# Optimization experiments

Measured on AMD Instinct MI355X. Metric: run time of the kernel, lower is better.

The kernel has to match this reference:

```python
import jax, jax.numpy as jnp
import numpy as np

B = 256      # number of graphs
IN = 128     # input_dim
FD = 256     # feature_dim (dims[1])
HID = 256    # hidden_dim of attention block (dims[2])
OUT = 128    # final output dim (dims[3])
TXT = 512    # text_emb_dim

LENGTHS = np.asarray(128 + (np.arange(B) % 256), dtype=np.int64)  # ragged lens 128..383
N = int(LENGTHS.sum())  # 65408 total nodes
LMAX = int(LENGTHS.max())  # 383


def setup_inputs() -> dict:
    key = jax.random.key(0)
    ks = jax.random.split(key, 16)
    s = 0.02
    return {
        "input": jax.random.normal(ks[0], (N, IN), jnp.float32),
        "text_emb": jax.random.normal(ks[1], (B, TXT), jnp.float32),
        "repeat_list": jnp.asarray(LENGTHS),
        # layer 0: Linear(IN -> FD)
        "W0": jax.random.normal(ks[2], (IN, FD), jnp.float32) * s,
        "b0": jax.random.normal(ks[3], (FD,), jnp.float32) * s,
        # cross-attention block params
        "Wq": jax.random.normal(ks[4], (TXT, FD), jnp.float32) * s,
        "bq": jax.random.normal(ks[5], (FD,), jnp.float32) * s,
        "Wk": jax.random.normal(ks[6], (FD, FD), jnp.float32) * s,
        "bk": jax.random.normal(ks[7], (FD,), jnp.float32) * s,
        "Wv": jax.random.normal(ks[8], (FD, FD), jnp.float32) * s,
        "bv": jax.random.normal(ks[9], (FD,), jnp.float32) * s,
        "Wo": jax.random.normal(ks[10], (FD, HID), jnp.float32) * s,
        "bo": jax.random.normal(ks[11], (HID,), jnp.float32) * s,
        # layer 2: Linear(HID -> OUT), last layer (no activation)
        "W2": jax.random.normal(ks[12], (HID, OUT), jnp.float32) * s,
        "b2": jax.random.normal(ks[13], (OUT,), jnp.float32) * s,
    }


def _cross_attention(h, text_emb, repeat_list, Wq, bq, Wk, bk, Wv, bv, Wo, bo):
    # h: [N, FD] packed ragged node features; repeat_list: [B] lengths (constant ints)
    n = h.shape[0]
    b = repeat_list.shape[0]
    fd = h.shape[1]
    # pad ragged -> [B, LMAX, FD] (pad value 0) + validity mask
    seg = jnp.repeat(jnp.arange(b), repeat_list, total_repeat_length=n)  # [N] graph id
    offsets = jnp.cumsum(repeat_list) - repeat_list                      # [B] start of each graph
    pos = jnp.arange(n) - offsets[seg]                                   # [N] within-graph pos
    padded = jnp.zeros((b, LMAX, fd), h.dtype).at[seg, pos].set(h)
    valid = jnp.arange(LMAX)[None, :] < repeat_list[:, None]             # [B, L]

    q = text_emb @ Wq + bq                              # [B, FD]
    k = (padded @ Wk + bk) * valid[..., None]           # masked_fill(mask==0, 0)
    v = (padded @ Wv + bv) * valid[..., None]

    # query is broadcast identically over the padded-length axis, so each row of the
    # [L, L] score matrix is the same vector: scores[b, j] = q[b] . k[b, j]
    scores = jnp.einsum('bf,bjf->bj', q, k)             # [B, L]
    scores = jnp.where(valid, scores, -jnp.inf)         # mask invalid columns j
    p = jax.nn.softmax(scores, axis=-1)                 # [B, L]
    # output = attention^T @ value with identical rows => out[b,j,:] = p[b,j] * sum_i v[b,i,:]
    v_sum = v.sum(axis=1)                               # [B, FD] (padded rows already zero)
    out_pad = p[..., None] * v_sum[:, None, :]          # [B, L, FD]
    out_nodes = out_pad[seg, pos]                       # unpad-concat -> [N, FD]
    return out_nodes @ Wo + bo                          # [N, HID]


def reference(input, text_emb, repeat_list, W0, b0, Wq, bq, Wk, bk, Wv, bv, Wo, bo, W2, b2):
    h = jax.nn.relu(input @ W0 + b0)                                     # layer 0 + relu
    h = _cross_attention(h, text_emb, repeat_list, Wq, bq, Wk, bk, Wv, bv, Wo, bo)
    h = jax.nn.relu(h)                                                   # layer 1 + relu
    return h @ W2 + b2                                                   # layer 2 (last, no act)
```

## Files before the change

### kernel.cpp

```cpp
#include <hip/hip_runtime.h>
#include <math.h>

#define B_G   256
#define IN_D  128
#define FD    256
#define HID   256
#define OUT_D 128
#define TXT   512
#define XKS   136
#define ZKS   72

typedef short bf16x8 __attribute__((ext_vector_type(8)));
typedef float f32x4  __attribute__((ext_vector_type(4)));

__device__ __forceinline__ unsigned bf_rne(float x) {
    unsigned u = __float_as_uint(x);
    u += 0x7fffu + ((u >> 16) & 1u);
    return u >> 16;
}
__device__ __forceinline__ float bf_to_f(unsigned h) {
    return __uint_as_float(h << 16);
}
__device__ __forceinline__ void split2(float a0, float a1, unsigned& hp, unsigned& lp) {
    unsigned h0 = bf_rne(a0), h1 = bf_rne(a1);
    float r0 = a0 - bf_to_f(h0), r1 = a1 - bf_to_f(h1);
    hp = h0 | (h1 << 16);
    lp = bf_rne(r0) | (bf_rne(r1) << 16);
}

__global__ __launch_bounds__(256) void k_prepA(
    const float* __restrict__ text_emb, const float* __restrict__ Wq,
    const float* __restrict__ bq, const float* __restrict__ Wk,
    const float* __restrict__ W0, const float* __restrict__ W2,
    const int* __restrict__ lens,
    float* __restrict__ qk, int* __restrict__ offsets, float* __restrict__ hsum,
    unsigned short* __restrict__ W0sH, unsigned short* __restrict__ W0sL,
    unsigned short* __restrict__ W2sH, unsigned short* __restrict__ W2sL)
{
    int blk = blockIdx.x, t = threadIdx.x;
    __shared__ float te[TXT];
    __shared__ float q[FD];
    __shared__ int   sc[B_G];

    if (blk < 256) {
        int b = blk;
        hsum[b * FD + t] = 0.f;
        for (int i = t; i < TXT; i += 256) te[i] = text_emb[(size_t)b * TXT + i];
        __syncthreads();
        float acc = bq[t];
        for (int k = 0; k < TXT; k++) acc = fmaf(te[k], Wq[k * FD + t], acc);
        q[t] = acc;
        __syncthreads();
        float a2 = 0.f;
        for (int f = 0; f < FD; f++) a2 = fmaf(Wk[t * FD + f], q[f], a2);
        qk[b * FD + t] = a2;
    } else if (blk < 264) {
        int e = (blk - 256) * 256 + t;
        if (e < 1024) {
            int kc = e >> 8, c = e & 255;
            size_t base = (size_t)(kc * 256 + c) * 32;
            for (int kk = 0; kk < 32; kk++) {
                float v = W0[(size_t)(kc * 32 + kk) * FD + c];
                unsigned h = bf_rne(v);
                float r = v - bf_to_f(h);
                W0sH[base + kk] = (unsigned short)h;
                W0sL[base + kk] = (unsigned short)bf_rne(r);
            }
        } else {
            int e2 = e - 1024;
            int kc = e2 >> 7, c = e2 & 127;
            size_t base = (size_t)(kc * 128 + c) * 32;
            for (int kk = 0; kk < 32; kk++) {
                float v = W2[(size_t)(kc * 32 + kk) * OUT_D + c];
                unsigned h = bf_rne(v);
                float r = v - bf_to_f(h);
                W2sH[base + kk] = (unsigned short)h;
                W2sL[base + kk] = (unsigned short)bf_rne(r);
            }
        }
    } else {
        sc[t] = lens[t];
        __syncthreads();
        for (int d = 1; d < 256; d <<= 1) {
            int v = (t >= d) ? sc[t - d] : 0;
            __syncthreads();
            sc[t] += v;
            __syncthreads();
        }
        offsets[t + 1] = sc[t];
        if (t == 0) offsets[0] = 0;
    }
}

__global__ __launch_bounds__(256, 3) void k_l0_mfma(
    const float* __restrict__ X,
    const unsigned short* __restrict__ W0sH, const unsigned short* __restrict__ W0sL,
    const float* __restrict__ b0, const float* __restrict__ qk,
    const int* __restrict__ offsets,
    float* __restrict__ scores, float* __restrict__ hsum)
{
    int b = blockIdx.y;
    int off = offsets[b], len = offsets[b + 1] - off;
    int n0 = blockIdx.x * 64;
    if (n0 >= len) return;
    int nvalid = min(64, len - n0);

    __shared__ __align__(16) unsigned short XsH[64 * XKS], XsL[64 * XKS];
    __shared__ float qks[FD];
    __shared__ float bsh[FD];
    __shared__ float red[4][64];

    int tid = threadIdx.x;
    int lane = tid & 63, w = tid >> 6;
    int ln = lane & 15, quad = lane >> 4;

    qks[tid] = qk[b * FD + tid];
    bsh[tid] = b0[tid];

    {
        int node_s = tid >> 2, ks = (tid & 3) * 32;
        const float* Xr = X + (size_t)(off + n0 + node_s) * IN_D + ks;
        float xv[32];
        if (node_s < nvalid) {
#pragma unroll
            for (int q2 = 0; q2 < 8; q2++) {
                float4 v = ((const float4*)Xr)[q2];
                xv[q2 * 4 + 0] = v.x; xv[q2 * 4 + 1] = v.y;
                xv[q2 * 4 + 2] = v.z; xv[q2 * 4 + 3] = v.w;
            }
        } else {
#pragma unroll
            for (int q2 = 0; q2 < 32; q2++) xv[q2] = 0.f;
        }
#pragma unroll
        for (int g = 0; g < 4; g++) {
            uint4 hq, lq;
            split2(xv[g * 8 + 0], xv[g * 8 + 1], hq.x, lq.x);
            split2(xv[g * 8 + 2], xv[g * 8 + 3], hq.y, lq.y);
            split2(xv[g * 8 + 4], xv[g * 8 + 5], hq.z, lq.z);
            split2(xv[g * 8 + 6], xv[g * 8 + 7], hq.w, lq.w);
            *(uint4*)&XsH[node_s * XKS + ks + g * 8] = hq;
            *(uint4*)&XsL[node_s * XKS + ks + g * 8] = lq;
        }
    }
    __syncthreads();

    f32x4 acc[4][4] = {};
#pragma unroll
    for (int kc = 0; kc < 4; kc++) {
        bf16x8 AH[4], AL[4], BH[4], BL[4];
#pragma unroll
        for (int i = 0; i < 4; i++) {
            AH[i] = *(const bf16x8*)&XsH[(16 * i + ln) * XKS + kc * 32 + quad * 8];
            AL[i] = *(const bf16x8*)&XsL[(16 * i + ln) * XKS + kc * 32 + quad * 8];
        }
#pragma unroll
        for (int j = 0; j < 4; j++) {
            int c = 64 * w + 16 * j + ln;
            size_t base = (size_t)(kc * 256 + c) * 32 + quad * 8;
            BH[j] = *(const bf16x8*)&W0sH[base];
            BL[j] = *(const bf16x8*)&W0sL[base];
        }
#pragma unroll
        for (int i = 0; i < 4; i++)
#pragma unroll
            for (int j = 0; j < 4; j++) {
                acc[i][j] = __builtin_amdgcn_mfma_f32_16x16x32_bf16(AH[i], BH[j], acc[i][j], 0, 0, 0);
                acc[i][j] = __builtin_amdgcn_mfma_f32_16x16x32_bf16(AH[i], BL[j], acc[i][j], 0, 0, 0);
                acc[i][j] = __builtin_amdgcn_mfma_f32_16x16x32_bf16(AL[i], BH[j], acc[i][j], 0, 0, 0);
            }
    }

    float sp[4][4];
    float cs[4] = {0.f, 0.f, 0.f, 0.f};
#pragma unroll
    for (int i = 0; i < 4; i++)
#pragma unroll
        for (int r = 0; r < 4; r++) sp[i][r] = 0.f;

#pragma unroll
    for (int i = 0; i < 4; i++)
#pragma unroll
        for (int j = 0; j < 4; j++) {
            int c = 64 * w + 16 * j + ln;
            float bb = bsh[c], qv = qks[c];
#pragma unroll
            for (int r = 0; r < 4; r++) {
                int node = 16 * i + 4 * quad + r;
                float h = acc[i][j][r] + bb;
                h = (h > 0.f && node < nvalid) ? h : 0.f;
                sp[i][r] = fmaf(h, qv, sp[i][r]);
                cs[j] += h;
            }
        }
#pragma unroll
    for (int i = 0; i < 4; i++)
#pragma unroll
        for (int r = 0; r < 4; r++) {
            float s = sp[i][r];
            s += __shfl_xor(s, 1); s += __shfl_xor(s, 2);
            s += __shfl_xor(s, 4); s += __shfl_xor(s, 8);
            sp[i][r] = s;
        }
    if (ln == 0) {
#pragma unroll
        for (int i = 0; i < 4; i++)
#pragma unroll
            for (int r = 0; r < 4; r++)
                red[w][16 * i + 4 * quad + r] = sp[i][r];
    }
#pragma unroll
    for (int j = 0; j < 4; j++) {
        float s = cs[j];
        s += __shfl_xor(s, 16); s += __shfl_xor(s, 32);
        if (quad == 0) atomicAdd(&hsum[b * FD + 64 * w + 16 * j + ln], s);
    }
    __syncthreads();
    if (tid < 64 && tid < nvalid)
        scores[off + n0 + tid] = red[0][tid] + red[1][tid] + red[2][tid] + red[3][tid];
}

__global__ __launch_bounds__(1024) void k_graph(
    const float* __restrict__ scores, const float* __restrict__ hsum,
    const float* __restrict__ Wv, const float* __restrict__ bv,
    const float* __restrict__ Wo, const int* __restrict__ offsets,
    float* __restrict__ wvec, float* __restrict__ smax, float* __restrict__ dinv)
{
    int b = blockIdx.x, tid = threadIdx.x;
    int t = tid & 255, g = tid >> 8;
    int off = offsets[b], len = offsets[b + 1] - off;
    __shared__ float redm[16], reds[16];
    __shared__ float hs[FD], vs[FD];
    __shared__ float part[4][FD];

    float m = -INFINITY;
    for (int i = tid; i < len; i += 1024) m = fmaxf(m, scores[off + i]);
    for (int d = 1; d < 64; d <<= 1) m = fmaxf(m, __shfl_xor(m, d));
    if ((tid & 63) == 0) redm[tid >> 6] = m;
    __syncthreads();
    m = -INFINITY;
#pragma unroll
    for (int k = 0; k < 16; k++) m = fmaxf(m, redm[k]);

    float s = 0.f;
    for (int i = tid; i < len; i += 1024) s += expf(scores[off + i] - m);
    for (int d = 1; d < 64; d <<= 1) s += __shfl_xor(s, d);
    if ((tid & 63) == 0) reds[tid >> 6] = s;
    if (g == 0) hs[t] = hsum[b * FD + t];
    __syncthreads();
    s = 0.f;
#pragma unroll
    for (int k = 0; k < 16; k++) s += reds[k];

    float acc = (g == 0) ? (float)len * bv[t] : 0.f;
    for (int f = 64 * g; f < 64 * g + 64; f++) acc = fmaf(hs[f], Wv[f * FD + t], acc);
    part[g][t] = acc;
    __syncthreads();
    if (g == 0) vs[t] = part[0][t] + part[1][t] + part[2][t] + part[3][t];
    __syncthreads();
    float a2 = 0.f;
    for (int f = 64 * g; f < 64 * g + 64; f++) a2 = fmaf(vs[f], Wo[f * HID + t], a2);
    part[g][t] = a2;
    __syncthreads();
    if (g == 0) wvec[b * HID + t] = part[0][t] + part[1][t] + part[2][t] + part[3][t];
    if (tid == 0) { smax[b] = m; dinv[b] = 1.0f / s; }
}

__global__ __launch_bounds__(256, 5) void k_fin_mfma(
    const float* __restrict__ scores, const float* __restrict__ wvec,
    const float* __restrict__ bo,
    const unsigned short* __restrict__ W2sH, const unsigned short* __restrict__ W2sL,
    const float* __restrict__ b2, const float* __restrict__ smax,
    const float* __restrict__ dinv, const int* __restrict__ offsets,
    float* __restrict__ Y)
{
    int b = blockIdx.y;
    int off = offsets[b], len = offsets[b + 1] - off;
    int n0 = blockIdx.x * 64;
    if (n0 >= len) return;
    int nvalid = min(64, len - n0);

    int tid = threadIdx.x;
    int lane = tid & 63, w = tid >> 6;
    int ln = lane & 15, quad = lane >> 4;

    __shared__ __align__(16) unsigned short ZsH[64 * ZKS], ZsL[64 * ZKS];
    __shared__ float ps[64];
    __shared__ __align__(16) float wsh[HID];
    __shared__ __align__(16) float bosh[HID];
    __shared__ float b2sh[OUT_D];

    wsh[tid] = wvec[b * HID + tid];
    bosh[tid] = bo[tid];
    if (tid < OUT_D) b2sh[tid] = b2[tid];
    if (tid < 64) {
        float p = 0.f;
        if (tid < nvalid) p = expf(scores[off + n0 + tid] - smax[b]) * dinv[b];
        ps[tid] = p;
    }
    __syncthreads();

    f32x4 acc[4][2] = {};
    int node_s = tid >> 2, ks = (tid & 3) * 16;

#pragma unroll
    for (int s = 0; s < 4; s++) {
        if (s) __syncthreads();
        {
            float pn = ps[node_s];
#pragma unroll
            for (int g = 0; g < 2; g++) {
                int kl = ks + g * 8;
                int kg = s * 64 + kl;
                float4 w4a = *(const float4*)&wsh[kg];
                float4 w4b = *(const float4*)&wsh[kg + 4];
                float4 b4a = *(const float4*)&bosh[kg];
                float4 b4b = *(const float4*)&bosh[kg + 4];
                uint4 hq, lq;
                float z0, z1;
                z0 = fmaxf(fmaf(pn, w4a.x, b4a.x), 0.f);
                z1 = fmaxf(fmaf(pn, w4a.y, b4a.y), 0.f);
                split2(z0, z1, hq.x, lq.x);
                z0 = fmaxf(fmaf(pn, w4a.z, b4a.z), 0.f);
                z1 = fmaxf(fmaf(pn, w4a.w, b4a.w), 0.f);
                split2(z0, z1, hq.y, lq.y);
                z0 = fmaxf(fmaf(pn, w4b.x, b4b.x), 0.f);
                z1 = fmaxf(fmaf(pn, w4b.y, b4b.y), 0.f);
                split2(z0, z1, hq.z, lq.z);
                z0 = fmaxf(fmaf(pn, w4b.z, b4b.z), 0.f);
                z1 = fmaxf(fmaf(pn, w4b.w, b4b.w), 0.f);
                split2(z0, z1, hq.w, lq.w);
                *(uint4*)&ZsH[node_s * ZKS + kl] = hq;
                *(uint4*)&ZsL[node_s * ZKS + kl] = lq;
            }
        }
        __syncthreads();

#pragma unroll
        for (int kc = 0; kc < 2; kc++) {
            bf16x8 AH[4], AL[4];
#pragma unroll
            for (int i = 0; i < 4; i++) {
                AH[i] = *(const bf16x8*)&ZsH[(16 * i + ln) * ZKS + kc * 32 + quad * 8];
                AL[i] = *(const bf16x8*)&ZsL[(16 * i + ln) * ZKS + kc * 32 + quad * 8];
            }
#pragma unroll
            for (int j = 0; j < 2; j++) {
                int c = 32 * w + 16 * j + ln;
                size_t base = (size_t)((s * 2 + kc) * 128 + c) * 32 + quad * 8;
                bf16x8 BH = *(const bf16x8*)&W2sH[base];
                bf16x8 BL = *(const bf16x8*)&W2sL[base];
#pragma unroll
                for (int i = 0; i < 4; i++) {
                    acc[i][j] = __builtin_amdgcn_mfma_f32_16x16x32_bf16(AH[i], BH, acc[i][j], 0, 0, 0);
                    acc[i][j] = __builtin_amdgcn_mfma_f32_16x16x32_bf16(AH[i], BL, acc[i][j], 0, 0, 0);
                    acc[i][j] = __builtin_amdgcn_mfma_f32_16x16x32_bf16(AL[i], BH, acc[i][j], 0, 0, 0);
                }
            }
        }
    }

#pragma unroll
    for (int i = 0; i < 4; i++)
#pragma unroll
        for (int j = 0; j < 2; j++) {
            int c = 32 * w + 16 * j + ln;
            float bb = b2sh[c];
#pragma unroll
            for (int r = 0; r < 4; r++) {
                int node = 16 * i + 4 * quad + r;
                if (node < nvalid)
                    Y[(size_t)(off + n0 + node) * OUT_D + c] = acc[i][j][r] + bb;
            }
        }
}

extern "C" void kernel_launch(void* const* d_in, const int* in_sizes, int n_in,
                              void* d_out, int out_size, void* d_ws, size_t ws_size,
                              hipStream_t stream)
{
    const float* X        = (const float*)d_in[0];
    const float* text_emb = (const float*)d_in[1];
    const int*   lens     = (const int*)d_in[2];
    const float* W0       = (const float*)d_in[3];
    const float* b0       = (const float*)d_in[4];
    const float* Wq       = (const float*)d_in[5];
    const float* bq       = (const float*)d_in[6];
    const float* Wk       = (const float*)d_in[7];
    const float* Wv       = (const float*)d_in[9];
    const float* bv       = (const float*)d_in[10];
    const float* Wo       = (const float*)d_in[11];
    const float* bo       = (const float*)d_in[12];
    const float* W2       = (const float*)d_in[13];
    const float* b2       = (const float*)d_in[14];
    float* Y = (float*)d_out;

    char* base = (char*)d_ws;
    size_t o = 0;
    int*   offsets = (int*)(base + o);            o += 1088;
    float* qkbuf   = (float*)(base + o);          o += 262144;
    float* wvecb   = (float*)(base + o);          o += 262144;
    float* smaxb   = (float*)(base + o);          o += 1024;
    float* dinvb   = (float*)(base + o);          o += 1024;
    float* hsum    = (float*)(base + o);          o += 262144;
    float* scores  = (float*)(base + o);          o += 262144;
    unsigned short* W0sH = (unsigned short*)(base + o); o += 65536;
    unsigned short* W0sL = (unsigned short*)(base + o); o += 65536;
    unsigned short* W2sH = (unsigned short*)(base + o); o += 65536;
    unsigned short* W2sL = (unsigned short*)(base + o); o += 65536;

    k_prepA<<<265, 256, 0, stream>>>(text_emb, Wq, bq, Wk, W0, W2, lens,
                                     qkbuf, offsets, hsum, W0sH, W0sL, W2sH, W2sL);
    k_l0_mfma<<<dim3(6, B_G), 256, 0, stream>>>(X, W0sH, W0sL, b0, qkbuf, offsets, scores, hsum);
    k_graph<<<B_G, 1024, 0, stream>>>(scores, hsum, Wv, bv, Wo, offsets, wvecb, smaxb, dinvb);
    k_fin_mfma<<<dim3(6, B_G), 256, 0, stream>>>(scores, wvecb, bo, W2sH, W2sL, b2, smaxb, dinvb, offsets, Y);
}
```

Measured before the change: 186.3 us.

## Batch per-graph Wv/Wo matvecs into split-bf16 MFMA GEMMs in k_mid

Replaces the per-graph k_graph kernel, which did scalar fp32 matvecs of hsum through Wv and Wo with one 1024-thread block per graph, with k_mid. k_mid batches 16 graphs per block and runs both products as split-bf16 (hi/lo, 4 MFMAs) GEMMs, with Wv and Wo pre-split and pre-swizzled in the prep kernel. The softmax max/sum statistics move to separate 256-thread blocks in the same launch. The aim is to stop every graph re-reading the full Wv and Wo matrices and to use matrix cores, at the cost of extra prep work, extra workspace, and approximation error from the bf16 split.

```diff
diff --git a/kernel.cpp b/kernel.cpp
--- a/kernel.cpp
+++ b/kernel.cpp
@@ -9,6 +9,7 @@
 #define TXT   512
 #define XKS   136
 #define ZKS   72
+#define MKS   264
 
 typedef short bf16x8 __attribute__((ext_vector_type(8)));
 typedef float f32x4  __attribute__((ext_vector_type(4)));
@@ -32,10 +33,13 @@
     const float* __restrict__ text_emb, const float* __restrict__ Wq,
     const float* __restrict__ bq, const float* __restrict__ Wk,
     const float* __restrict__ W0, const float* __restrict__ W2,
+    const float* __restrict__ Wv, const float* __restrict__ Wo,
     const int* __restrict__ lens,
     float* __restrict__ qk, int* __restrict__ offsets, float* __restrict__ hsum,
     unsigned short* __restrict__ W0sH, unsigned short* __restrict__ W0sL,
-    unsigned short* __restrict__ W2sH, unsigned short* __restrict__ W2sL)
+    unsigned short* __restrict__ W2sH, unsigned short* __restrict__ W2sL,
+    unsigned short* __restrict__ WvsH, unsigned short* __restrict__ WvsL,
+    unsigned short* __restrict__ WosH, unsigned short* __restrict__ WosL)
 {
     int blk = blockIdx.x, t = threadIdx.x;
     __shared__ float te[TXT];
@@ -78,6 +82,28 @@
                 W2sL[base + kk] = (unsigned short)bf_rne(r);
             }
         }
+    } else if (blk < 272) {
+        int e = (blk - 264) * 256 + t;
+        int kc = e >> 8, c = e & 255;
+        size_t base = (size_t)(kc * 256 + c) * 32;
+        for (int kk = 0; kk < 32; kk++) {
+            float v = Wv[(size_t)(kc * 32 + kk) * FD + c];
+            unsigned h = bf_rne(v);
+            float r = v - bf_to_f(h);
+            WvsH[base + kk] = (unsigned short)h;
+            WvsL[base + kk] = (unsigned short)bf_rne(r);
+        }
+    } else if (blk < 280) {
+        int e = (blk - 272) * 256 + t;
+        int kc = e >> 8, c = e & 255;
+        size_t base = (size_t)(kc * 256 + c) * 32;
+        for (int kk = 0; kk < 32; kk++) {
+            float v = Wo[(size_t)(kc * 32 + kk) * HID + c];
+            unsigned h = bf_rne(v);
+            float r = v - bf_to_f(h);
+            WosH[base + kk] = (unsigned short)h;
+            WosL[base + kk] = (unsigned short)bf_rne(r);
+        }
     } else {
         sc[t] = lens[t];
         __syncthreads();
@@ -220,50 +246,126 @@
         scores[off + n0 + tid] = red[0][tid] + red[1][tid] + red[2][tid] + red[3][tid];
 }
 
-__global__ __launch_bounds__(1024) void k_graph(
+__global__ __launch_bounds__(256) void k_mid(
     const float* __restrict__ scores, const float* __restrict__ hsum,
-    const float* __restrict__ Wv, const float* __restrict__ bv,
-    const float* __restrict__ Wo, const int* __restrict__ offsets,
+    const unsigned short* __restrict__ WvsH, const unsigned short* __restrict__ WvsL,
+    const unsigned short* __restrict__ WosH, const unsigned short* __restrict__ WosL,
+    const float* __restrict__ bv, const int* __restrict__ offsets,
     float* __restrict__ wvec, float* __restrict__ smax, float* __restrict__ dinv)
 {
-    int b = blockIdx.x, tid = threadIdx.x;
-    int t = tid & 255, g = tid >> 8;
-    int off = offsets[b], len = offsets[b + 1] - off;
-    __shared__ float redm[16], reds[16];
-    __shared__ float hs[FD], vs[FD];
-    __shared__ float part[4][FD];
-
-    float m = -INFINITY;
-    for (int i = tid; i < len; i += 1024) m = fmaxf(m, scores[off + i]);
-    for (int d = 1; d < 64; d <<= 1) m = fmaxf(m, __shfl_xor(m, d));
-    if ((tid & 63) == 0) redm[tid >> 6] = m;
+    int blk = blockIdx.x, tid = threadIdx.x;
+    int lane = tid & 63, w = tid >> 6;
+
+    __shared__ __align__(16) unsigned short AsH[16 * MKS], AsL[16 * MKS];
+    __shared__ float lensh[16];
+    __shared__ float redm[4], reds[4];
+
+    if (blk >= 16) {
+        int b = blk - 16;
+        int off = offsets[b], len = offsets[b + 1] - off;
+        float s0 = (tid < len) ? scores[off + tid] : -INFINITY;
+        float s1 = (tid + 256 < len) ? scores[off + tid + 256] : -INFINITY;
+        float m = fmaxf(s0, s1);
+#pragma unroll
+        for (int d = 1; d < 64; d <<= 1) m = fmaxf(m, __shfl_xor(m, d));
+        if (lane == 0) redm[w] = m;
+        __syncthreads();
+        m = fmaxf(fmaxf(redm[0], redm[1]), fmaxf(redm[2], redm[3]));
+        float e = ((tid < len) ? expf(s0 - m) : 0.f)
+                + ((tid + 256 < len) ? expf(s1 - m) : 0.f);
+#pragma unroll
+        for (int d = 1; d < 64; d <<= 1) e += __shfl_xor(e, d);
+        if (lane == 0) reds[w] = e;
+        __syncthreads();
+        float s = reds[0] + reds[1] + reds[2] + reds[3];
+        if (tid == 0) { smax[b] = m; dinv[b] = 1.0f / s; }
+        return;
+    }
+
+    int g0 = blk * 16;
+    int ln = lane & 15, quad = lane >> 4;
+
+    if (tid < 16) lensh[tid] = (float)(offsets[g0 + tid + 1] - offsets[g0 + tid]);
+
+    {
+        int row = tid >> 4, ks = (tid & 15) * 16;
+        const float4* H4 = (const float4*)(hsum + (size_t)(g0 + row) * FD + ks);
+#pragma unroll
+        for (int g = 0; g < 2; g++) {
+            float4 a = H4[2 * g], c4 = H4[2 * g + 1];
+            uint4 hq, lq;
+            split2(a.x,  a.y,  hq.x, lq.x);
+            split2(a.z,  a.w,  hq.y, lq.y);
+            split2(c4.x, c4.y, hq.z, lq.z);
+            split2(c4.z, c4.w, hq.w, lq.w);
+            *(uint4*)&AsH[row * MKS + ks + g * 8] = hq;
+            *(uint4*)&AsL[row * MKS + ks + g * 8] = lq;
+        }
+    }
     __syncthreads();
-    m = -INFINITY;
-#pragma unroll
-    for (int k = 0; k < 16; k++) m = fmaxf(m, redm[k]);
-
-    float s = 0.f;
-    for (int i = tid; i < len; i += 1024) s += expf(scores[off + i] - m);
-    for (int d = 1; d < 64; d <<= 1) s += __shfl_xor(s, d);
-    if ((tid & 63) == 0) reds[tid >> 6] = s;
-    if (g == 0) hs[t] = hsum[b * FD + t];
+
+    f32x4 acc[4] = {};
+#pragma unroll
+    for (int kc = 0; kc < 8; kc++) {
+        bf16x8 AH = *(const bf16x8*)&AsH[ln * MKS + kc * 32 + quad * 8];
+        bf16x8 AL = *(const bf16x8*)&AsL[ln * MKS + kc * 32 + quad * 8];
+#pragma unroll
+        for (int j = 0; j < 4; j++) {
+            int c = 64 * w + 16 * j + ln;
+            size_t base = (size_t)(kc * 256 + c) * 32 + quad * 8;
+            bf16x8 BH = *(const bf16x8*)&WvsH[base];
+            bf16x8 BL = *(const bf16x8*)&WvsL[base];
+            acc[j] = __builtin_amdgcn_mfma_f32_16x16x32_bf16(AH, BH, acc[j], 0, 0, 0);
+            acc[j] = __builtin_amdgcn_mfma_f32_16x16x32_bf16(AH, BL, acc[j], 0, 0, 0);
+            acc[j] = __builtin_amdgcn_mfma_f32_16x16x32_bf16(AL, BH, acc[j], 0, 0, 0);
+            acc[j] = __builtin_amdgcn_mfma_f32_16x16x32_bf16(AL, BL, acc[j], 0, 0, 0);
+        }
+    }
     __syncthreads();
-    s = 0.f;
-#pragma unroll
-    for (int k = 0; k < 16; k++) s += reds[k];
-
-    float acc = (g == 0) ? (float)len * bv[t] : 0.f;
-    for (int f = 64 * g; f < 64 * g + 64; f++) acc = fmaf(hs[f], Wv[f * FD + t], acc);
-    part[g][t] = acc;
+
+#pragma unroll
+    for (int j = 0; j < 4; j++) {
+        int c = 64 * w + 16 * j + ln;
+        float bvv = bv[c];
+#pragma unroll
+        for (int r = 0; r < 4; r++) {
+            int row = 4 * quad + r;
+            float v = acc[j][r] + lensh[row] * bvv;
+            unsigned h = bf_rne(v);
+            float res = v - bf_to_f(h);
+            AsH[row * MKS + c] = (unsigned short)h;
+            AsL[row * MKS + c] = (unsigned short)bf_rne(res);
+        }
+    }
     __syncthreads();
-    if (g == 0) vs[t] = part[0][t] + part[1][t] + part[2][t] + part[3][t];
-    __syncthreads();
-    float a2 = 0.f;
-    for (int f = 64 * g; f < 64 * g + 64; f++) a2 = fmaf(vs[f], Wo[f * HID + t], a2);
-    part[g][t] = a2;
-    __syncthreads();
-    if (g == 0) wvec[b * HID + t] = part[0][t] + part[1][t] + part[2][t] + part[3][t];
-    if (tid == 0) { smax[b] = m; dinv[b] = 1.0f / s; }
+
+    f32x4 acc2[4] = {};
+#pragma unroll
+    for (int kc = 0; kc < 8; kc++) {
+        bf16x8 AH = *(const bf16x8*)&AsH[ln * MKS + kc * 32 + quad * 8];
+        bf16x8 AL = *(const bf16x8*)&AsL[ln * MKS + kc * 32 + quad * 8];
+#pragma unroll
+        for (int j = 0; j < 4; j++) {
+            int c = 64 * w + 16 * j + ln;
+            size_t base = (size_t)(kc * 256 + c) * 32 + quad * 8;
+            bf16x8 BH = *(const bf16x8*)&WosH[base];
+            bf16x8 BL = *(const bf16x8*)&WosL[base];
+            acc2[j] = __builtin_amdgcn_mfma_f32_16x16x32_bf16(AH, BH, acc2[j], 0, 0, 0);
+            acc2[j] = __builtin_amdgcn_mfma_f32_16x16x32_bf16(AH, BL, acc2[j], 0, 0, 0);
+            acc2[j] = __builtin_amdgcn_mfma_f32_16x16x32_bf16(AL, BH, acc2[j], 0, 0, 0);
+            acc2[j] = __builtin_amdgcn_mfma_f32_16x16x32_bf16(AL, BL, acc2[j], 0, 0, 0);
+        }
+    }
+
+#pragma unroll
+    for (int j = 0; j < 4; j++) {
+        int c = 64 * w + 16 * j + ln;
+#pragma unroll
+        for (int r = 0; r < 4; r++) {
+            int row = 4 * quad + r;
+            wvec[(size_t)(g0 + row) * HID + c] = acc2[j][r];
+        }
+    }
 }
 
 __global__ __launch_bounds__(256, 5) void k_fin_mfma(
@@ -408,10 +510,16 @@
     unsigned short* W0sL = (unsigned short*)(base + o); o += 65536;
     unsigned short* W2sH = (unsigned short*)(base + o); o += 65536;
     unsigned short* W2sL = (unsigned short*)(base + o); o += 65536;
-
-    k_prepA<<<265, 256, 0, stream>>>(text_emb, Wq, bq, Wk, W0, W2, lens,
-                                     qkbuf, offsets, hsum, W0sH, W0sL, W2sH, W2sL);
+    unsigned short* WvsH = (unsigned short*)(base + o); o += 131072;
+    unsigned short* WvsL = (unsigned short*)(base + o); o += 131072;
+    unsigned short* WosH = (unsigned short*)(base + o); o += 131072;
+    unsigned short* WosL = (unsigned short*)(base + o); o += 131072;
+
+    k_prepA<<<281, 256, 0, stream>>>(text_emb, Wq, bq, Wk, W0, W2, Wv, Wo, lens,
+                                     qkbuf, offsets, hsum,
+                                     W0sH, W0sL, W2sH, W2sL, WvsH, WvsL, WosH, WosL);
     k_l0_mfma<<<dim3(6, B_G), 256, 0, stream>>>(X, W0sH, W0sL, b0, qkbuf, offsets, scores, hsum);
-    k_graph<<<B_G, 1024, 0, stream>>>(scores, hsum, Wv, bv, Wo, offsets, wvecb, smaxb, dinvb);
+    k_mid<<<272, 256, 0, stream>>>(scores, hsum, WvsH, WvsL, WosH, WosL, bv, offsets,
+                                   wvecb, smaxb, dinvb);
     k_fin_mfma<<<dim3(6, B_G), 256, 0, stream>>>(scores, wvecb, bo, W2sH, W2sL, b2, smaxb, dinvb, offsets, Y);
 }
```

After: 185.4 us. About the same (-0.5%).
